# Kernel tuning notes

Measured on AMD Instinct MI355X. Metric: run time of the kernel, lower is better.

## Reference

```python
import jax, jax.numpy as jnp
import numpy as np

N = 50000          # nodes
DEG = 16           # out-degree
E = N * DEG        # edges
IN = 256           # input feature dim
H = 8              # hidden heads
DH = 32            # per-head hidden dim (hidden_dim // H)
HID = H * DH       # 256
OUT = 64           # output dim (single output head)
ALPHA = 0.2        # LeakyReLU negative slope


def _xavier(k, shape, fan_in, fan_out):
    limit = 1.414 * np.sqrt(6.0 / (fan_in + fan_out))
    return jax.random.uniform(k, shape, jnp.float32, -limit, limit)


def setup_inputs() -> dict:
    key = jax.random.key(0)
    ks = jax.random.split(key, 6)
    X = jax.random.normal(ks[0], (N, IN), jnp.float32)
    src = jnp.repeat(jnp.arange(N, dtype=jnp.int32), DEG)      # every row non-empty
    dst = jax.random.randint(ks[1], (E,), 0, N, jnp.int32)
    edges = jnp.stack([src, dst])                               # [2, E]
    W0 = _xavier(ks[2], (H, IN, DH), IN, DH)
    a0 = _xavier(ks[3], (H, 2 * DH), 2 * DH, 1)
    W1 = _xavier(ks[4], (1, HID, OUT), HID, OUT)
    a1 = _xavier(ks[5], (1, 2 * OUT), 2 * OUT, 1)
    return {"X": X, "edges": edges, "W0": W0, "a0": a0, "W1": W1, "a1": a1}


def sparse_gat_layer(X, edges, W, a):
    # W: [H, Din, D], a: [H, 2D]. Equivalent to concat(h_src, h_dst) @ a split.
    n = X.shape[0]
    D = W.shape[2]
    src, dst = edges[0], edges[1]
    h = jnp.einsum('nd,hde->hne', X, W)                         # [H, N, D]
    s_src = jnp.einsum('hne,he->hn', h, a[:, :D])               # [H, N]
    s_dst = jnp.einsum('hne,he->hn', h, a[:, D:])               # [H, N]
    e = jax.nn.leaky_relu(s_src[:, src] + s_dst[:, dst], ALPHA)  # [H, E]
    # stable per-row (segment = src) softmax, matching torch.sparse.softmax(dim=1)
    seg_max = jax.lax.stop_gradient(
        jax.vmap(lambda v: jax.ops.segment_max(v, src, num_segments=n))(e))
    p = jnp.exp(e - seg_max[:, src])
    denom = jax.vmap(lambda v: jax.ops.segment_sum(v, src, num_segments=n))(p)
    att = p / denom[:, src]                                      # [H, E]
    # out[i] = sum_{e: src=i} att_e * h[dst_e]
    agg = jax.vmap(lambda a_, hh: jax.ops.segment_sum(a_[:, None] * hh[dst], src,
                                                      num_segments=n))(att, h)
    return agg                                                   # [H, N, D]


def reference(X, edges, W0, a0, W1, a1):
    h1 = jax.nn.elu(sparse_gat_layer(X, edges, W0, a0))          # [H, N, DH]
    X1 = jnp.transpose(h1, (1, 0, 2)).reshape(X.shape[0], -1)    # concat heads [N, HID]
    out = sparse_gat_layer(X1, edges, W1, a1)                    # [1, N, OUT]
    return jax.nn.elu(out[0])                                    # num_heads_out = 1
```

## Files before the change

kernel.cpp:

```cpp
#include <hip/hip_runtime.h>

typedef __attribute__((ext_vector_type(8))) short bh8;
typedef __attribute__((ext_vector_type(4))) float f4;

static __device__ __forceinline__ float b2f(unsigned short u){
  union { unsigned int i; float f; } c; c.i = ((unsigned int)u) << 16; return c.f;
}
static __device__ __forceinline__ unsigned short f2b(float f){
  union { float f; unsigned int i; } c; c.f = f;
  unsigned int u = c.i; u += 0x7fffu + ((u >> 16) & 1u);
  return (unsigned short)(u >> 16);
}
static __device__ __forceinline__ float elu1(float x){ return x > 0.f ? x : (__expf(x) - 1.f); }
static __device__ __forceinline__ float lrelu(float x){ return x > 0.f ? x : 0.2f * x; }
static __device__ __forceinline__ float gload(const void* p, size_t i, int isf32){
  return isf32 ? ((const float*)p)[i] : b2f(((const unsigned short*)p)[i]);
}

__global__ void detect_kernel(const unsigned int* __restrict__ W0w, int* __restrict__ flag){
  __shared__ int cnt;
  int tid = threadIdx.x;
  if (tid == 0) cnt = 0;
  __syncthreads();
  unsigned int w = W0w[tid];
  unsigned int e = (w >> 7) & 0xFFu;
  int plaus = (e >= 100u && e <= 126u) ? 1 : 0;
  atomicAdd(&cnt, plaus);
  __syncthreads();
  if (tid == 0) flag[0] = (cnt >= 64) ? 0 : 1;
}

__global__ __launch_bounds__(256) void prep_kernel(
    const void* __restrict__ W0, const void* __restrict__ a0,
    const void* __restrict__ W1, const void* __restrict__ a1,
    unsigned short* __restrict__ Wt1, unsigned short* __restrict__ Wt2,
    const int* __restrict__ flagp){
  int isf = *flagp;
  int c = blockIdx.x, k = threadIdx.x;
  if (c < 272){
    float v;
    if (c < 256){
      int h = c >> 5, d = c & 31;
      v = gload(W0, (size_t)(h*256 + k)*32 + d, isf);
    } else if (c < 264){
      int h = c - 256; float s = 0.f;
      for (int d = 0; d < 32; d++)
        s += gload(W0, (size_t)(h*256 + k)*32 + d, isf) * gload(a0, h*64 + d, isf);
      v = s;
    } else {
      int h = c - 264; float s = 0.f;
      for (int d = 0; d < 32; d++)
        s += gload(W0, (size_t)(h*256 + k)*32 + d, isf) * gload(a0, h*64 + 32 + d, isf);
      v = s;
    }
    Wt1[c*256 + k] = f2b(v);
  } else {
    int c2 = c - 272; float v;
    if (c2 < 64) v = gload(W1, k*64 + c2, isf);
    else if (c2 == 64){ float s = 0.f; for (int i = 0; i < 64; i++) s += gload(W1, k*64+i, isf) * gload(a1, i, isf);      v = s; }
    else if (c2 == 65){ float s = 0.f; for (int i = 0; i < 64; i++) s += gload(W1, k*64+i, isf) * gload(a1, 64 + i, isf); v = s; }
    else v = 0.f;
    Wt2[c2*256 + k] = f2b(v);
  }
}

__global__ __launch_bounds__(64, 2) void gemm1_mfma(
    const void* __restrict__ Xraw, const unsigned short* __restrict__ Wt,
    unsigned short* __restrict__ H1, float* __restrict__ S1, int N,
    const int* __restrict__ flagp){
  __shared__ __align__(16) unsigned short lds[32*264];
  int isf = *flagp;
  int lane = threadIdx.x;
  int q = lane >> 4, l = lane & 15;
  int n0 = blockIdx.x*32;
  int r0 = n0 + l;      if (r0 > N-1) r0 = N-1;
  int r1 = n0 + 16 + l; if (r1 > N-1) r1 = N-1;
  bh8 a0[8], a1[8];
  if (isf){
    const float* x0 = (const float*)Xraw + (size_t)r0*256;
    const float* x1 = (const float*)Xraw + (size_t)r1*256;
    #pragma unroll
    for (int kk = 0; kk < 8; kk++){
      int base = kk*32 + q*8;
      float4 u0 = *(const float4*)(x0 + base), u1 = *(const float4*)(x0 + base + 4);
      bh8 t;
      t[0]=(short)f2b(u0.x); t[1]=(short)f2b(u0.y); t[2]=(short)f2b(u0.z); t[3]=(short)f2b(u0.w);
      t[4]=(short)f2b(u1.x); t[5]=(short)f2b(u1.y); t[6]=(short)f2b(u1.z); t[7]=(short)f2b(u1.w);
      a0[kk] = t;
      float4 v0 = *(const float4*)(x1 + base), v1 = *(const float4*)(x1 + base + 4);
      t[0]=(short)f2b(v0.x); t[1]=(short)f2b(v0.y); t[2]=(short)f2b(v0.z); t[3]=(short)f2b(v0.w);
      t[4]=(short)f2b(v1.x); t[5]=(short)f2b(v1.y); t[6]=(short)f2b(v1.z); t[7]=(short)f2b(v1.w);
      a1[kk] = t;
    }
  } else {
    const bh8* x0 = (const bh8*)((const unsigned short*)Xraw + (size_t)r0*256);
    const bh8* x1 = (const bh8*)((const unsigned short*)Xraw + (size_t)r1*256);
    #pragma unroll
    for (int kk = 0; kk < 8; kk++){ a0[kk] = x0[kk*4 + q]; a1[kk] = x1[kk*4 + q]; }
  }
  const bh8* Wb = (const bh8*)Wt;
  bh8 bc[8], bn[8];
  #pragma unroll
  for (int kk = 0; kk < 8; kk++) bc[kk] = Wb[(size_t)l*32 + kk*4 + q];
  for (int t = 0; t < 17; t++){
    if (t < 16){
      #pragma unroll
      for (int kk = 0; kk < 8; kk++) bn[kk] = Wb[(size_t)((t+1)*16 + l)*32 + kk*4 + q];
    }
    f4 c0 = {0.f,0.f,0.f,0.f}, c1 = {0.f,0.f,0.f,0.f};
    #pragma unroll
    for (int kk = 0; kk < 8; kk++){
      c0 = __builtin_amdgcn_mfma_f32_16x16x32_bf16(a0[kk], bc[kk], c0, 0, 0, 0);
      c1 = __builtin_amdgcn_mfma_f32_16x16x32_bf16(a1[kk], bc[kk], c1, 0, 0, 0);
    }
    if (t < 16){
      #pragma unroll
      for (int r = 0; r < 4; r++){
        lds[(q*4 + r)*264 + t*16 + l]      = f2b(c0[r]);
        lds[(16 + q*4 + r)*264 + t*16 + l] = f2b(c1[r]);
      }
      #pragma unroll
      for (int kk = 0; kk < 8; kk++) bc[kk] = bn[kk];
    } else {
      #pragma unroll
      for (int r = 0; r < 4; r++){
        int row0 = n0 + q*4 + r, row1 = n0 + 16 + q*4 + r;
        if (row0 < N) S1[(size_t)row0*16 + l] = c0[r];
        if (row1 < N) S1[(size_t)row1*16 + l] = c1[r];
      }
    }
  }
  __syncthreads();
  int ch = lane & 31;
  #pragma unroll
  for (int g = 0; g < 16; g++){
    int r2 = g*2 + (lane >> 5);
    int row = n0 + r2;
    if (row < N)
      *(bh8*)(H1 + (size_t)row*256 + ch*8) = *(const bh8*)&lds[r2*264 + ch*8];
  }
}

__global__ __launch_bounds__(64, 2) void gemm2_mfma(
    const unsigned short* __restrict__ X1, const unsigned short* __restrict__ Wt,
    unsigned short* __restrict__ H2, float* __restrict__ S2, int N){
  __shared__ __align__(16) unsigned short lds[32*72];
  int lane = threadIdx.x;
  int q = lane >> 4, l = lane & 15;
  int n0 = blockIdx.x*32;
  int r0 = n0 + l;      if (r0 > N-1) r0 = N-1;
  int r1 = n0 + 16 + l; if (r1 > N-1) r1 = N-1;
  const bh8* x0 = (const bh8*)(X1 + (size_t)r0*256);
  const bh8* x1 = (const bh8*)(X1 + (size_t)r1*256);
  bh8 a0[8], a1[8];
  #pragma unroll
  for (int kk = 0; kk < 8; kk++){ a0[kk] = x0[kk*4 + q]; a1[kk] = x1[kk*4 + q]; }
  const bh8* Wb = (const bh8*)Wt;
  bh8 bc[8], bn[8];
  #pragma unroll
  for (int kk = 0; kk < 8; kk++) bc[kk] = Wb[(size_t)l*32 + kk*4 + q];
  for (int t = 0; t < 5; t++){
    if (t < 4){
      #pragma unroll
      for (int kk = 0; kk < 8; kk++) bn[kk] = Wb[(size_t)((t+1)*16 + l)*32 + kk*4 + q];
    }
    f4 c0 = {0.f,0.f,0.f,0.f}, c1 = {0.f,0.f,0.f,0.f};
    #pragma unroll
    for (int kk = 0; kk < 8; kk++){
      c0 = __builtin_amdgcn_mfma_f32_16x16x32_bf16(a0[kk], bc[kk], c0, 0, 0, 0);
      c1 = __builtin_amdgcn_mfma_f32_16x16x32_bf16(a1[kk], bc[kk], c1, 0, 0, 0);
    }
    if (t < 4){
      #pragma unroll
      for (int r = 0; r < 4; r++){
        lds[(q*4 + r)*72 + t*16 + l]      = f2b(c0[r]);
        lds[(16 + q*4 + r)*72 + t*16 + l] = f2b(c1[r]);
      }
      #pragma unroll
      for (int kk = 0; kk < 8; kk++) bc[kk] = bn[kk];
    } else if (l < 2){
      #pragma unroll
      for (int r = 0; r < 4; r++){
        int row0 = n0 + q*4 + r, row1 = n0 + 16 + q*4 + r;
        if (row0 < N) S2[(size_t)row0*2 + l] = c0[r];
        if (row1 < N) S2[(size_t)row1*2 + l] = c1[r];
      }
    }
  }
  __syncthreads();
  int ch = lane & 7;
  #pragma unroll
  for (int g = 0; g < 4; g++){
    int r2 = g*8 + (lane >> 3);
    int row = n0 + r2;
    if (row < N)
      *(bh8*)(H2 + (size_t)row*64 + ch*8) = *(const bh8*)&lds[r2*72 + ch*8];
  }
}

__global__ __launch_bounds__(256) void agg1_kernel(
    const float* __restrict__ S1, const unsigned short* __restrict__ H1,
    const int* __restrict__ dst, unsigned short* __restrict__ X1, int N){
  __shared__ float att[4][128];
  __shared__ int dl[4][16];
  int tid = threadIdx.x, wv = tid >> 6, lane = tid & 63;
  int node = blockIdx.x*4 + wv; if (node > N-1) node = N-1;
  int h = lane >> 3, jj = lane & 7;
  const int* dp = dst + (size_t)node*16;
  int d0 = dp[jj], d1 = dp[jj + 8];
  float ss = S1[(size_t)node*16 + h];
  float e0 = lrelu(ss + S1[(size_t)d0*16 + 8 + h]);
  float e1 = lrelu(ss + S1[(size_t)d1*16 + 8 + h]);
  float m = fmaxf(e0, e1);
  m = fmaxf(m, __shfl_xor(m, 1)); m = fmaxf(m, __shfl_xor(m, 2)); m = fmaxf(m, __shfl_xor(m, 4));
  float p0 = __expf(e0 - m), p1 = __expf(e1 - m);
  float s = p0 + p1;
  s += __shfl_xor(s, 1); s += __shfl_xor(s, 2); s += __shfl_xor(s, 4);
  float inv = 1.f / s;
  att[wv][h*16 + jj]     = p0 * inv;
  att[wv][h*16 + jj + 8] = p1 * inv;
  if (h == 0){ dl[wv][jj] = d0; dl[wv][jj + 8] = d1; }
  __syncthreads();
  int cb = lane*4, hb = lane >> 3;
  float c0 = 0.f, c1 = 0.f, c2 = 0.f, c3 = 0.f;
  #pragma unroll
  for (int j = 0; j < 16; j++){
    float aw = att[wv][hb*16 + j];
    int dd = dl[wv][j];
    ushort4 v = *(const ushort4*)(H1 + (size_t)dd*256 + cb);
    c0 += aw * b2f(v.x); c1 += aw * b2f(v.y); c2 += aw * b2f(v.z); c3 += aw * b2f(v.w);
  }
  ushort4 o;
  o.x = f2b(elu1(c0)); o.y = f2b(elu1(c1)); o.z = f2b(elu1(c2)); o.w = f2b(elu1(c3));
  *(ushort4*)(X1 + (size_t)node*256 + cb) = o;
}

__global__ __launch_bounds__(256) void agg2_kernel(
    const float* __restrict__ S2, const unsigned short* __restrict__ H2,
    const int* __restrict__ dst, void* __restrict__ outv, int N,
    const int* __restrict__ flagp){
  __shared__ float att[4][16];
  __shared__ int dl[4][16];
  int isf = *flagp;
  int tid = threadIdx.x, wv = tid >> 6, lane = tid & 63;
  int node = blockIdx.x*4 + wv; if (node > N-1) node = N-1;
  int j = lane & 15;
  int d = dst[(size_t)node*16 + j];
  float e = lrelu(S2[(size_t)node*2] + S2[(size_t)d*2 + 1]);
  float m = e;
  m = fmaxf(m, __shfl_xor(m, 1)); m = fmaxf(m, __shfl_xor(m, 2));
  m = fmaxf(m, __shfl_xor(m, 4)); m = fmaxf(m, __shfl_xor(m, 8));
  float p = __expf(e - m);
  float s = p;
  s += __shfl_xor(s, 1); s += __shfl_xor(s, 2); s += __shfl_xor(s, 4); s += __shfl_xor(s, 8);
  if (lane < 16){ att[wv][j] = p / s; dl[wv][j] = d; }
  __syncthreads();
  float acc = 0.f;
  #pragma unroll
  for (int t = 0; t < 16; t++)
    acc += att[wv][t] * b2f(H2[(size_t)dl[wv][t]*64 + lane]);
  float v = elu1(acc);
  size_t oi = (size_t)node*64 + lane;
  if (isf) ((float*)outv)[oi] = v;
  else     ((unsigned short*)outv)[oi] = f2b(v);
}

extern "C" void kernel_launch(void* const* d_in, const int* in_sizes, int n_in,
                              void* d_out, int out_size, void* d_ws, size_t ws_size,
                              hipStream_t stream){
  const void* X  = d_in[0];
  const int*  ed = (const int*)d_in[1];
  const void* W0 = d_in[2];
  const void* a0 = d_in[3];
  const void* W1 = d_in[4];
  const void* a1 = d_in[5];

  int N = in_sizes[0] / 256;
  int E = N * 16;
  const int* dst = ed + E;

  char* w = (char*)d_ws;
  size_t off = 0;
  auto alloc = [&](size_t bytes) -> void* {
    void* p = w + off; off += (bytes + 255) & ~(size_t)255; return p;
  };
  int*            flag = (int*)alloc(4);
  unsigned short* Wt1  = (unsigned short*)alloc(272*256*2);
  unsigned short* Wt2  = (unsigned short*)alloc(80*256*2);
  float*          S1   = (float*)alloc((size_t)N*16*4);
  unsigned short* H1   = (unsigned short*)alloc((size_t)N*256*2);
  unsigned short* X1   = (unsigned short*)alloc((size_t)N*256*2);
  unsigned short* H2   = H1;
  float*          S2   = (float*)(H1 + (size_t)N*64);
  (void)ws_size; (void)n_in; (void)out_size;

  int gb = (N + 31) / 32;
  int ab = (N + 3) / 4;
  detect_kernel <<<1,  128, 0, stream>>>((const unsigned int*)W0, flag);
  prep_kernel   <<<352,256, 0, stream>>>(W0, a0, W1, a1, Wt1, Wt2, flag);
  gemm1_mfma    <<<gb, 64,  0, stream>>>(X,  Wt1, H1, S1, N, flag);
  agg1_kernel   <<<ab, 256, 0, stream>>>(S1, H1, dst, X1, N);
  gemm2_mfma    <<<gb, 64,  0, stream>>>(X1, Wt2, H2, S2, N);
  agg2_kernel   <<<ab, 256, 0, stream>>>(S2, H2, dst, d_out, N, flag);
}
```

Before: 232.3 us.

## Fuse layer-1 aggregation with layer-2 GEMM via LDS and vectorize agg2 gathers

The layer-1 attention aggregation and the layer-2 MFMA GEMM now run in one kernel. Each 256-thread block aggregates 32 nodes into an LDS tile, then its four waves compute the H2/S2 projections straight from LDS, so the X1 intermediate no longer makes a round trip through HBM and one launch is dropped. agg2 now gathers 8 bf16 values per lane using shuffles instead of an LDS staging buffer with a barrier, then reduces across lane groups. The cost is a serial 8-node aggregation loop per wave and an uneven split of the GEMM across waves, since wave 3 computes two tiles.

After: 227.7 us. 1.02x faster.

```diff
diff --git a/kernel.cpp b/kernel.cpp
--- a/kernel.cpp
+++ b/kernel.cpp
@@ -141,106 +141,103 @@
   }
 }
 
-__global__ __launch_bounds__(64, 2) void gemm2_mfma(
-    const unsigned short* __restrict__ X1, const unsigned short* __restrict__ Wt,
+__global__ __launch_bounds__(256) void fused_agg1_gemm2(
+    const float* __restrict__ S1, const unsigned short* __restrict__ H1,
+    const int* __restrict__ dst, const unsigned short* __restrict__ Wt2,
     unsigned short* __restrict__ H2, float* __restrict__ S2, int N){
-  __shared__ __align__(16) unsigned short lds[32*72];
-  int lane = threadIdx.x;
-  int q = lane >> 4, l = lane & 15;
+  __shared__ __align__(16) unsigned short Xt[32*264];
+  __shared__ __align__(16) unsigned short Hs[32*88];
+  int tid = threadIdx.x, wv = tid >> 6, lane = tid & 63;
   int n0 = blockIdx.x*32;
-  int r0 = n0 + l;      if (r0 > N-1) r0 = N-1;
-  int r1 = n0 + 16 + l; if (r1 > N-1) r1 = N-1;
-  const bh8* x0 = (const bh8*)(X1 + (size_t)r0*256);
-  const bh8* x1 = (const bh8*)(X1 + (size_t)r1*256);
-  bh8 a0[8], a1[8];
-  #pragma unroll
-  for (int kk = 0; kk < 8; kk++){ a0[kk] = x0[kk*4 + q]; a1[kk] = x1[kk*4 + q]; }
-  const bh8* Wb = (const bh8*)Wt;
-  bh8 bc[8], bn[8];
-  #pragma unroll
-  for (int kk = 0; kk < 8; kk++) bc[kk] = Wb[(size_t)l*32 + kk*4 + q];
-  for (int t = 0; t < 5; t++){
-    if (t < 4){
-      #pragma unroll
-      for (int kk = 0; kk < 8; kk++) bn[kk] = Wb[(size_t)((t+1)*16 + l)*32 + kk*4 + q];
-    }
-    f4 c0 = {0.f,0.f,0.f,0.f}, c1 = {0.f,0.f,0.f,0.f};
+  int h = lane >> 3, jj = lane & 7;
+  int half = lane >> 5, li = lane & 31;
+  int cb = li*8, hc = li >> 2;
+  for (int ni = 0; ni < 8; ni++){
+    int lrow = wv*8 + ni;
+    int node = n0 + lrow; if (node > N-1) node = N-1;
+    const int* dp = dst + (size_t)node*16;
+    int d0 = dp[jj], d1 = dp[jj + 8];
+    float ss = S1[(size_t)node*16 + h];
+    float e0 = lrelu(ss + S1[(size_t)d0*16 + 8 + h]);
+    float e1 = lrelu(ss + S1[(size_t)d1*16 + 8 + h]);
+    float m = fmaxf(e0, e1);
+    m = fmaxf(m, __shfl_xor(m, 1)); m = fmaxf(m, __shfl_xor(m, 2)); m = fmaxf(m, __shfl_xor(m, 4));
+    float p0 = __expf(e0 - m), p1 = __expf(e1 - m);
+    float s = p0 + p1;
+    s += __shfl_xor(s, 1); s += __shfl_xor(s, 2); s += __shfl_xor(s, 4);
+    float inv = 1.f / s;
+    float v0a = p0 * inv, v1a = p1 * inv;
+    float acc[8] = {0.f,0.f,0.f,0.f,0.f,0.f,0.f,0.f};
+    #pragma unroll
+    for (int i = 0; i < 8; i++){
+      int j  = i*2 + half;
+      int jl = j & 7;
+      int row  = (i < 4) ? __shfl(d0,  jl) : __shfl(d1,  jl);
+      float aw = (i < 4) ? __shfl(v0a, hc*8 + jl) : __shfl(v1a, hc*8 + jl);
+      bh8 v = *(const bh8*)(H1 + (size_t)row*256 + cb);
+      #pragma unroll
+      for (int c = 0; c < 8; c++) acc[c] += aw * b2f((unsigned short)v[c]);
+    }
+    #pragma unroll
+    for (int c = 0; c < 8; c++) acc[c] += __shfl_xor(acc[c], 32);
+    if (half == 0){
+      bh8 o;
+      #pragma unroll
+      for (int c = 0; c < 8; c++) o[c] = (short)f2b(elu1(acc[c]));
+      *(bh8*)&Xt[lrow*264 + cb] = o;
+    }
+  }
+  __syncthreads();
+  {
+    int q = lane >> 4, l = lane & 15;
+    bh8 a0[8], a1[8];
     #pragma unroll
     for (int kk = 0; kk < 8; kk++){
-      c0 = __builtin_amdgcn_mfma_f32_16x16x32_bf16(a0[kk], bc[kk], c0, 0, 0, 0);
-      c1 = __builtin_amdgcn_mfma_f32_16x16x32_bf16(a1[kk], bc[kk], c1, 0, 0, 0);
-    }
-    if (t < 4){
-      #pragma unroll
-      for (int r = 0; r < 4; r++){
-        lds[(q*4 + r)*72 + t*16 + l]      = f2b(c0[r]);
-        lds[(16 + q*4 + r)*72 + t*16 + l] = f2b(c1[r]);
+      a0[kk] = *(const bh8*)&Xt[l*264 + kk*32 + q*8];
+      a1[kk] = *(const bh8*)&Xt[(16 + l)*264 + kk*32 + q*8];
+    }
+    const bh8* Wb = (const bh8*)Wt2;
+    int ntt = (wv == 3) ? 2 : 1;
+    for (int it = 0; it < ntt; it++){
+      int tt = (it == 0) ? wv : 4;
+      bh8 b[8];
+      #pragma unroll
+      for (int kk = 0; kk < 8; kk++) b[kk] = Wb[(size_t)(tt*16 + l)*32 + kk*4 + q];
+      f4 c0 = {0.f,0.f,0.f,0.f}, c1 = {0.f,0.f,0.f,0.f};
+      #pragma unroll
+      for (int kk = 0; kk < 8; kk++){
+        c0 = __builtin_amdgcn_mfma_f32_16x16x32_bf16(a0[kk], b[kk], c0, 0, 0, 0);
+        c1 = __builtin_amdgcn_mfma_f32_16x16x32_bf16(a1[kk], b[kk], c1, 0, 0, 0);
       }
-      #pragma unroll
-      for (int kk = 0; kk < 8; kk++) bc[kk] = bn[kk];
-    } else if (l < 2){
-      #pragma unroll
-      for (int r = 0; r < 4; r++){
-        int row0 = n0 + q*4 + r, row1 = n0 + 16 + q*4 + r;
-        if (row0 < N) S2[(size_t)row0*2 + l] = c0[r];
-        if (row1 < N) S2[(size_t)row1*2 + l] = c1[r];
+      if (tt < 4){
+        #pragma unroll
+        for (int r = 0; r < 4; r++){
+          Hs[(q*4 + r)*88 + tt*16 + l]      = f2b(c0[r]);
+          Hs[(16 + q*4 + r)*88 + tt*16 + l] = f2b(c1[r]);
+        }
+      } else if (l < 2){
+        #pragma unroll
+        for (int r = 0; r < 4; r++){
+          int row0 = n0 + q*4 + r, row1 = n0 + 16 + q*4 + r;
+          if (row0 < N) S2[(size_t)row0*2 + l] = c0[r];
+          if (row1 < N) S2[(size_t)row1*2 + l] = c1[r];
+        }
       }
     }
   }
   __syncthreads();
-  int ch = lane & 7;
-  #pragma unroll
-  for (int g = 0; g < 4; g++){
-    int r2 = g*8 + (lane >> 3);
+  {
+    int r2 = tid >> 3, ch = tid & 7;
     int row = n0 + r2;
     if (row < N)
-      *(bh8*)(H2 + (size_t)row*64 + ch*8) = *(const bh8*)&lds[r2*72 + ch*8];
-  }
-}
-
-__global__ __launch_bounds__(256) void agg1_kernel(
-    const float* __restrict__ S1, const unsigned short* __restrict__ H1,
-    const int* __restrict__ dst, unsigned short* __restrict__ X1, int N){
-  __shared__ float att[4][128];
-  __shared__ int dl[4][16];
-  int tid = threadIdx.x, wv = tid >> 6, lane = tid & 63;
-  int node = blockIdx.x*4 + wv; if (node > N-1) node = N-1;
-  int h = lane >> 3, jj = lane & 7;
-  const int* dp = dst + (size_t)node*16;
-  int d0 = dp[jj], d1 = dp[jj + 8];
-  float ss = S1[(size_t)node*16 + h];
-  float e0 = lrelu(ss + S1[(size_t)d0*16 + 8 + h]);
-  float e1 = lrelu(ss + S1[(size_t)d1*16 + 8 + h]);
-  float m = fmaxf(e0, e1);
-  m = fmaxf(m, __shfl_xor(m, 1)); m = fmaxf(m, __shfl_xor(m, 2)); m = fmaxf(m, __shfl_xor(m, 4));
-  float p0 = __expf(e0 - m), p1 = __expf(e1 - m);
-  float s = p0 + p1;
-  s += __shfl_xor(s, 1); s += __shfl_xor(s, 2); s += __shfl_xor(s, 4);
-  float inv = 1.f / s;
-  att[wv][h*16 + jj]     = p0 * inv;
-  att[wv][h*16 + jj + 8] = p1 * inv;
-  if (h == 0){ dl[wv][jj] = d0; dl[wv][jj + 8] = d1; }
-  __syncthreads();
-  int cb = lane*4, hb = lane >> 3;
-  float c0 = 0.f, c1 = 0.f, c2 = 0.f, c3 = 0.f;
-  #pragma unroll
-  for (int j = 0; j < 16; j++){
-    float aw = att[wv][hb*16 + j];
-    int dd = dl[wv][j];
-    ushort4 v = *(const ushort4*)(H1 + (size_t)dd*256 + cb);
-    c0 += aw * b2f(v.x); c1 += aw * b2f(v.y); c2 += aw * b2f(v.z); c3 += aw * b2f(v.w);
-  }
-  ushort4 o;
-  o.x = f2b(elu1(c0)); o.y = f2b(elu1(c1)); o.z = f2b(elu1(c2)); o.w = f2b(elu1(c3));
-  *(ushort4*)(X1 + (size_t)node*256 + cb) = o;
+      *(bh8*)(H2 + (size_t)row*64 + ch*8) = *(const bh8*)&Hs[r2*88 + ch*8];
+  }
 }
 
 __global__ __launch_bounds__(256) void agg2_kernel(
     const float* __restrict__ S2, const unsigned short* __restrict__ H2,
     const int* __restrict__ dst, void* __restrict__ outv, int N,
     const int* __restrict__ flagp){
-  __shared__ float att[4][16];
-  __shared__ int dl[4][16];
   int isf = *flagp;
   int tid = threadIdx.x, wv = tid >> 6, lane = tid & 63;
   int node = blockIdx.x*4 + wv; if (node > N-1) node = N-1;
@@ -253,16 +250,39 @@
   float p = __expf(e - m);
   float s = p;
   s += __shfl_xor(s, 1); s += __shfl_xor(s, 2); s += __shfl_xor(s, 4); s += __shfl_xor(s, 8);
-  if (lane < 16){ att[wv][j] = p / s; dl[wv][j] = d; }
-  __syncthreads();
-  float acc = 0.f;
+  float attv = p / s;
+  int g = lane >> 3, cbl = (lane & 7)*8;
+  float acc[8] = {0.f,0.f,0.f,0.f,0.f,0.f,0.f,0.f};
   #pragma unroll
-  for (int t = 0; t < 16; t++)
-    acc += att[wv][t] * b2f(H2[(size_t)dl[wv][t]*64 + lane]);
-  float v = elu1(acc);
-  size_t oi = (size_t)node*64 + lane;
-  if (isf) ((float*)outv)[oi] = v;
-  else     ((unsigned short*)outv)[oi] = f2b(v);
+  for (int it = 0; it < 2; it++){
+    int j2 = it*8 + g;
+    float aw = __shfl(attv, j2);
+    int row  = __shfl(d,    j2);
+    bh8 v = *(const bh8*)(H2 + (size_t)row*64 + cbl);
+    #pragma unroll
+    for (int c = 0; c < 8; c++) acc[c] += aw * b2f((unsigned short)v[c]);
+  }
+  #pragma unroll
+  for (int c = 0; c < 8; c++){
+    acc[c] += __shfl_xor(acc[c], 8);
+    acc[c] += __shfl_xor(acc[c], 16);
+    acc[c] += __shfl_xor(acc[c], 32);
+  }
+  if (lane < 8){
+    size_t oi = (size_t)node*64 + cbl;
+    if (isf){
+      float4 f0, f1;
+      f0.x = elu1(acc[0]); f0.y = elu1(acc[1]); f0.z = elu1(acc[2]); f0.w = elu1(acc[3]);
+      f1.x = elu1(acc[4]); f1.y = elu1(acc[5]); f1.z = elu1(acc[6]); f1.w = elu1(acc[7]);
+      *(float4*)((float*)outv + oi)     = f0;
+      *(float4*)((float*)outv + oi + 4) = f1;
+    } else {
+      bh8 o;
+      #pragma unroll
+      for (int c = 0; c < 8; c++) o[c] = (short)f2b(elu1(acc[c]));
+      *(bh8*)((unsigned short*)outv + oi) = o;
+    }
+  }
 }
 
 extern "C" void kernel_launch(void* const* d_in, const int* in_sizes, int n_in,
@@ -289,17 +309,15 @@
   unsigned short* Wt2  = (unsigned short*)alloc(80*256*2);
   float*          S1   = (float*)alloc((size_t)N*16*4);
   unsigned short* H1   = (unsigned short*)alloc((size_t)N*256*2);
-  unsigned short* X1   = (unsigned short*)alloc((size_t)N*256*2);
-  unsigned short* H2   = H1;
-  float*          S2   = (float*)(H1 + (size_t)N*64);
+  unsigned short* H2   = (unsigned short*)alloc((size_t)N*64*2);
+  float*          S2   = (float*)alloc((size_t)N*2*4);
   (void)ws_size; (void)n_in; (void)out_size;
 
   int gb = (N + 31) / 32;
   int ab = (N + 3) / 4;
-  detect_kernel <<<1,  128, 0, stream>>>((const unsigned int*)W0, flag);
-  prep_kernel   <<<352,256, 0, stream>>>(W0, a0, W1, a1, Wt1, Wt2, flag);
-  gemm1_mfma    <<<gb, 64,  0, stream>>>(X,  Wt1, H1, S1, N, flag);
-  agg1_kernel   <<<ab, 256, 0, stream>>>(S1, H1, dst, X1, N);
-  gemm2_mfma    <<<gb, 64,  0, stream>>>(X1, Wt2, H2, S2, N);
-  agg2_kernel   <<<ab, 256, 0, stream>>>(S2, H2, dst, d_out, N, flag);
-}
+  detect_kernel   <<<1,  128, 0, stream>>>((const unsigned int*)W0, flag);
+  prep_kernel     <<<352,256, 0, stream>>>(W0, a0, W1, a1, Wt1, Wt2, flag);
+  gemm1_mfma      <<<gb, 64,  0, stream>>>(X,  Wt1, H1, S1, N, flag);
+  fused_agg1_gemm2<<<gb, 256, 0, stream>>>(S1, H1, dst, Wt2, H2, S2, N);
+  agg2_kernel     <<<ab, 256, 0, stream>>>(S2, H2, dst, d_out, N, flag);
+}
```
